# Kernel optimization log

Measured on AMD Instinct MI355X. Metric: run time of the kernel, lower is better.

Reference implementation:

```python
import jax, jax.numpy as jnp
import numpy as np
import math

K = 7
B, C, H, W = 16, 3, 256, 256
N = 50000
ANGLE = 30.0; TRANS = 0.45; SHEAR = 0.3; SCALE0, SCALE1 = 1.0, 0.5  # self.scale assumed [1.0,0.5] (upstream AutoDO)


def _bilinear(img, xs, ys):
    # img: (C,Hs,Ws); xs,ys: (Ho,Wo) pixel coords; border padding (clamp)
    Cc, Hs, Ws = img.shape
    xs = jnp.clip(xs, 0.0, Ws - 1.0)
    ys = jnp.clip(ys, 0.0, Hs - 1.0)
    x0 = jnp.floor(xs); y0 = jnp.floor(ys)
    wx = xs - x0; wy = ys - y0
    x0i = x0.astype(jnp.int32); y0i = y0.astype(jnp.int32)
    x1i = jnp.minimum(x0i + 1, Ws - 1); y1i = jnp.minimum(y0i + 1, Hs - 1)
    Ia = img[:, y0i, x0i]; Ib = img[:, y0i, x1i]
    Ic = img[:, y1i, x0i]; Id = img[:, y1i, x1i]
    return Ia * (1 - wx) * (1 - wy) + Ib * wx * (1 - wy) + Ic * (1 - wx) * wy + Id * wx * wy


def _resize(x, Ho, Wo):
    # torch F.interpolate bilinear, align_corners=False, no antialias
    Bb, Cc, Hs, Ws = x.shape
    ys = (jnp.arange(Ho, dtype=x.dtype) + 0.5) * (Hs / Ho) - 0.5
    xs = (jnp.arange(Wo, dtype=x.dtype) + 0.5) * (Ws / Wo) - 0.5
    Y, X = jnp.meshgrid(ys, xs, indexing='ij')
    return jax.vmap(lambda im: _bilinear(im, X, Y))(x)


def _warp_perspective(x, M, Ho, Wo):
    # kornia.warp_perspective: dst(p) = src(M^-1 p), bilinear, border padding, align_corners=True
    Bb, Cc, Hs, Ws = x.shape
    Minv = jnp.linalg.inv(M)  # (B,3,3)
    yy, xx = jnp.meshgrid(jnp.arange(Ho, dtype=x.dtype), jnp.arange(Wo, dtype=x.dtype), indexing='ij')
    pts = jnp.stack([xx.ravel(), yy.ravel(), jnp.ones(Ho * Wo, dtype=x.dtype)])  # (3, Ho*Wo)
    src = jnp.einsum('bij,jn->bin', Minv, pts)
    xs = (src[:, 0] / src[:, 2]).reshape(Bb, Ho, Wo)
    ys = (src[:, 1] / src[:, 2]).reshape(Bb, Ho, Wo)
    return jax.vmap(_bilinear)(x, xs, ys)


def _forward(x, paramP, paramM, gumbel_u, eps, idx):
    dt = x.dtype
    pP = jax.nn.sigmoid(paramP[:, idx])  # (K,B)
    logits = jnp.stack([jnp.log(pP).ravel(), jnp.log(1.0 - pP).ravel()], axis=1)  # (K*B,2)
    g = -jnp.log(-jnp.log(gumbel_u))
    y_soft = jax.nn.softmax(logits + g, axis=1)  # tau=1
    y_hard = jax.nn.one_hot(jnp.argmax(y_soft, axis=1), 2, dtype=y_soft.dtype)
    y = y_hard + y_soft - jax.lax.stop_gradient(y_soft)  # straight-through hard gumbel
    sP = y[:, 0].reshape(K, B)
    sM = jax.nn.sigmoid(paramM[:, idx]) * eps  # (K,B)
    ang = sP[0] * sM[0] * ANGLE
    # replicate torch's cat(W//2 * ones(B), H//2 * ones(B)).view(-1,2) layout exactly
    ctr = jnp.concatenate([jnp.full((B,), W // 2, dt), jnp.full((B,), H // 2, dt)]).reshape(-1, 2)
    sx = SCALE0 + sP[5] * sM[5] * SCALE1
    sy = SCALE0 + sP[6] * sM[6] * SCALE1
    rad = jnp.deg2rad(ang); ca = jnp.cos(rad); sa = jnp.sin(rad)
    # kornia get_rotation_matrix2d: rot=[[c,s],[-s,c]] @ diag(sx,sy); t = ctr - rot@ctr
    sr = jnp.stack([jnp.stack([ca * sx, sa * sy], -1), jnp.stack([-sa * sx, ca * sy], -1)], -2)  # (B,2,2)
    t = ctr - jnp.einsum('bij,bj->bi', sr, ctr)
    eye = jnp.broadcast_to(jnp.eye(3, dtype=dt), (B, 3, 3))
    R = eye.at[:, :2, :2].set(sr).at[:, :2, 2].set(t)
    T = eye.at[:, 0, 2].set(W * sP[1] * sM[1] * TRANS).at[:, 1, 2].set(H * sP[2] * sM[2] * TRANS)
    S = eye.at[:, 0, 1].set(sP[3] * sM[3] * SHEAR).at[:, 1, 0].set(sP[4] * sM[4] * SHEAR)
    M = S @ T @ R
    x_up = _resize(x, 4 * H, 4 * W)
    x_w = _warp_perspective(x_up, M, 4 * H, 4 * W)
    return _resize(x_w, H, W)


def setup_inputs() -> dict:
    key = jax.random.key(0)
    k1, k2, k3, k4 = jax.random.split(key, 4)
    p = 1.0 / (K - 2)
    prob_logit = math.log(p / (1.0 - p))
    m = 5.0 / 10.0
    magn_logit = math.log(m / (1.0 - m))
    return {
        'x': jax.random.uniform(k1, (B, C, H, W), jnp.float32),
        'paramP': jnp.full((K, N), prob_logit, jnp.float32),
        'paramM': jnp.full((K, N), magn_logit, jnp.float32),
        'gumbel_u': jax.random.uniform(k2, (K * B, 2), jnp.float32, minval=1e-6, maxval=1.0 - 1e-6),
        'eps': jax.random.normal(k3, (K, B), jnp.float32),
        'idx': jax.random.randint(k4, (B,), 0, N, jnp.int32),
    }


def reference(x, paramP, paramM, gumbel_u, eps, idx):
    return _forward(x, paramP, paramM, gumbel_u, eps, idx)
```

## Files before the change

kernel.cpp:

```cpp
#include <hip/hip_runtime.h>
#include <math.h>


typedef float floatx4 __attribute__((ext_vector_type(4)));

__device__ __forceinline__ floatx4 load4(const float* p) {
    floatx4 v;
    __builtin_memcpy(&v, p, sizeof(v));
    return v;
}

struct Up { int i0; float w; };

__device__ __forceinline__ Up upc(int v) {
    float u = fmaf(0.25f, (float)v, -0.375f);
    u = fminf(fmaxf(u, 0.0f), 255.0f);
    float f = floorf(u);
    Up r; r.i0 = (int)f; r.w = u - f;
    return r;
}

struct Trip { float w0, w1, w2; int base; };

__device__ __forceinline__ Trip merged3(float s) {
    float f = floorf(s);
    float fr = s - f;
    int v0 = (int)f;
    int v1 = min(v0 + 1, 1023);
    Up c0 = upc(v0), c1 = upc(v1);
    float A0 = 1.0f - fr, A1 = fr;
    float b0 = A1 * (1.0f - c1.w), b1 = A1 * c1.w;
    bool d = (c1.i0 != c0.i0);
    Trip t;
    t.w0 = A0 * (1.0f - c0.w) + (d ? 0.0f : b0);
    t.w1 = A0 * c0.w + (d ? b0 : b1);
    t.w2 = d ? b1 : 0.0f;
    t.base = c0.i0;
    return t;
}

__device__ __forceinline__ void pair_accum(
    Trip cA, Trip cB, Trip rA, Trip rB,
    const float* __restrict__ xb, float* acc)
{
    int cb = min(cA.base, cB.base);
    int rb = min(rA.base, rB.base);
    float CA[4], CB[4], RA[4], RB[4];
    bool sa_ = (cA.base != cb);
    CA[0] = sa_ ? 0.f : cA.w0;  CA[1] = sa_ ? cA.w0 : cA.w1;
    CA[2] = sa_ ? cA.w1 : cA.w2;  CA[3] = sa_ ? cA.w2 : 0.f;
    bool sb_ = (cB.base != cb);
    CB[0] = sb_ ? 0.f : cB.w0;  CB[1] = sb_ ? cB.w0 : cB.w1;
    CB[2] = sb_ ? cB.w1 : cB.w2;  CB[3] = sb_ ? cB.w2 : 0.f;
    bool ra_ = (rA.base != rb);
    RA[0] = ra_ ? 0.f : rA.w0;  RA[1] = ra_ ? rA.w0 : rA.w1;
    RA[2] = ra_ ? rA.w1 : rA.w2;  RA[3] = ra_ ? rA.w2 : 0.f;
    bool rb_ = (rB.base != rb);
    RB[0] = rb_ ? 0.f : rB.w0;  RB[1] = rb_ ? rB.w0 : rB.w1;
    RB[2] = rb_ ? rB.w1 : rB.w2;  RB[3] = rb_ ? rB.w2 : 0.f;

    float W[4][4];
#pragma unroll
    for (int r = 0; r < 4; ++r)
#pragma unroll
        for (int c = 0; c < 4; ++c)
            W[r][c] = fmaf(RB[r], CB[c], RA[r] * CA[c]);

    int base = cb;
    if (cb > 252) {
        int shift = cb - 252;
        base = 252;
        for (int s = 0; s < shift; ++s) {
#pragma unroll
            for (int r = 0; r < 4; ++r) {
                W[r][3] = W[r][2]; W[r][2] = W[r][1];
                W[r][1] = W[r][0]; W[r][0] = 0.f;
            }
        }
    }
    int e0 = rb * 256 + base;
    int e1 = min(rb + 1, 255) * 256 + base;
    int e2 = min(rb + 2, 255) * 256 + base;
    int e3 = min(rb + 3, 255) * 256 + base;
#pragma unroll
    for (int ch = 0; ch < 3; ++ch) {
        const float* pc = xb + ch * 65536;
        floatx4 L0 = load4(pc + e0);
        floatx4 L1 = load4(pc + e1);
        floatx4 L2 = load4(pc + e2);
        floatx4 L3 = load4(pc + e3);
        float s0 = fmaf(W[0][3], L0.w, fmaf(W[0][2], L0.z, fmaf(W[0][1], L0.y, W[0][0] * L0.x)));
        float s1 = fmaf(W[1][3], L1.w, fmaf(W[1][2], L1.z, fmaf(W[1][1], L1.y, W[1][0] * L1.x)));
        float s2 = fmaf(W[2][3], L2.w, fmaf(W[2][2], L2.z, fmaf(W[2][1], L2.y, W[2][0] * L2.x)));
        float s3 = fmaf(W[3][3], L3.w, fmaf(W[3][2], L3.z, fmaf(W[3][1], L3.y, W[3][0] * L3.x)));
        acc[ch] += (s0 + s1) + (s2 + s3);
    }
}

__global__ __launch_bounds__(256) void fused_warp(
    const float* __restrict__ x,
    const float* __restrict__ paramP, const float* __restrict__ paramM,
    const float* __restrict__ gumbel_u, const float* __restrict__ eps,
    const int* __restrict__ idx,
    float* __restrict__ out, int N)
{
    __shared__ float smem[8];

    int b = blockIdx.z;
    int tid = threadIdx.y * 16 + threadIdx.x;

    if (tid < 64) {
        float dec = 0.f, sMv = 0.f;
        if (tid < 7) {
            int k = tid;
            int id = idx[b];
            float vP = paramP[k * N + id];
            float pP = 1.0f / (1.0f + expf(-vP));
            float l0 = logf(pP);
            float l1 = logf(1.0f - pP);
            float u0 = gumbel_u[(k * 16 + b) * 2 + 0];
            float u1 = gumbel_u[(k * 16 + b) * 2 + 1];
            float g0 = -logf(-logf(u0));
            float g1 = -logf(-logf(u1));
            dec = (l0 + g0 >= l1 + g1) ? 1.0f : 0.0f;
            float vM = paramM[k * N + id];
            float sig = 1.0f / (1.0f + expf(-vM));
            sMv = sig * eps[k * 16 + b];
        }
        float sP[7], sM[7];
#pragma unroll
        for (int k = 0; k < 7; ++k) {
            sP[k] = __shfl(dec, k, 64);
            sM[k] = __shfl(sMv, k, 64);
        }
        if (tid == 0) {
            float ang = sP[0] * sM[0] * 30.0f;
            float rad = ang * 0.017453292519943295f;
            float ca = cosf(rad), sa = sinf(rad);
            float sx = 1.0f + sP[5] * sM[5] * 0.5f;
            float sy = 1.0f + sP[6] * sM[6] * 0.5f;
            float sr00 = ca * sx, sr01 = sa * sy;
            float sr10 = -sa * sx, sr11 = ca * sy;
            float t0 = 128.0f - (sr00 + sr01) * 128.0f;
            float t1 = 128.0f - (sr10 + sr11) * 128.0f;
            float tx2 = 256.0f * sP[1] * sM[1] * 0.45f;
            float ty2 = 256.0f * sP[2] * sM[2] * 0.45f;
            float sh01 = sP[3] * sM[3] * 0.3f;
            float sh10 = sP[4] * sM[4] * 0.3f;
            float e0 = t0 + tx2, e1 = t1 + ty2;
            float a  = sr00 + sh01 * sr10;
            float bb = sr01 + sh01 * sr11;
            float txm = e0 + sh01 * e1;
            float c  = sh10 * sr00 + sr10;
            float d  = sh10 * sr01 + sr11;
            float tym = sh10 * e0 + e1;
            float det = a * d - bb * c;
            float rdet = 1.0f / det;
            smem[0] = d * rdet;
            smem[1] = -bb * rdet;
            smem[2] = (bb * tym - d * txm) * rdet;
            smem[3] = -c * rdet;
            smem[4] = a * rdet;
            smem[5] = (c * txm - a * tym) * rdet;
        }
    }
    __syncthreads();

    float m00 = smem[0], m01 = smem[1], m02 = smem[2];
    float m10 = smem[3], m11 = smem[4], m12 = smem[5];

    int wid  = tid >> 6;
    int lane = tid & 63;
    int lx = lane & 7, ly = lane >> 3;
    int j = blockIdx.x * 16 + ((wid & 1) * 8 + lx);
    int i = blockIdx.y * 16 + ((wid >> 1) * 8 + ly);

    const float* xb = x + b * 3 * 65536;

    float XA = (float)(4 * j + 1);
    float Y0 = (float)(4 * i + 1);
    float x0 = fmaf(m00, XA, fmaf(m01, Y0, m02));
    float y0 = fmaf(m10, XA, fmaf(m11, Y0, m12));
    float xs[4], ys[4];
    xs[0] = x0;        ys[0] = y0;
    xs[1] = x0 + m00;  ys[1] = y0 + m10;
    xs[2] = x0 + m01;  ys[2] = y0 + m11;
    xs[3] = xs[1] + m01; ys[3] = ys[1] + m11;

    Trip cx[4], ry[4];
#pragma unroll
    for (int s = 0; s < 4; ++s) {
        cx[s] = merged3(fminf(fmaxf(xs[s], 0.f), 1023.f));
        ry[s] = merged3(fminf(fmaxf(ys[s], 0.f), 1023.f));
    }

    int cbmin = min(min(cx[0].base, cx[1].base), min(cx[2].base, cx[3].base));
    int cbmax = max(max(cx[0].base, cx[1].base), max(cx[2].base, cx[3].base));
    int rbmin = min(min(ry[0].base, ry[1].base), min(ry[2].base, ry[3].base));
    int rbmax = max(max(ry[0].base, ry[1].base), max(ry[2].base, ry[3].base));

    float acc[3] = {0.f, 0.f, 0.f};

    if (((cbmax - cbmin) | (rbmax - rbmin)) <= 1) {
        float W[4][4];
#pragma unroll
        for (int s = 0; s < 4; ++s) {
            bool sc = (cx[s].base != cbmin);
            float C0 = sc ? 0.f : cx[s].w0;
            float C1 = sc ? cx[s].w0 : cx[s].w1;
            float C2 = sc ? cx[s].w1 : cx[s].w2;
            float C3 = sc ? cx[s].w2 : 0.f;
            bool sr = (ry[s].base != rbmin);
            float R0 = sr ? 0.f : ry[s].w0;
            float R1 = sr ? ry[s].w0 : ry[s].w1;
            float R2 = sr ? ry[s].w1 : ry[s].w2;
            float R3 = sr ? ry[s].w2 : 0.f;
            float C[4] = {C0, C1, C2, C3};
            float R[4] = {R0, R1, R2, R3};
            if (s == 0) {
#pragma unroll
                for (int r = 0; r < 4; ++r)
#pragma unroll
                    for (int c = 0; c < 4; ++c)
                        W[r][c] = R[r] * C[c];
            } else {
#pragma unroll
                for (int r = 0; r < 4; ++r)
#pragma unroll
                    for (int c = 0; c < 4; ++c)
                        W[r][c] = fmaf(R[r], C[c], W[r][c]);
            }
        }

        int base = cbmin;
        if (cbmin > 252) {
            int shift = cbmin - 252;
            base = 252;
            for (int s = 0; s < shift; ++s) {
#pragma unroll
                for (int r = 0; r < 4; ++r) {
                    W[r][3] = W[r][2]; W[r][2] = W[r][1];
                    W[r][1] = W[r][0]; W[r][0] = 0.f;
                }
            }
        }

        int e0 = rbmin * 256 + base;
        int e1 = min(rbmin + 1, 255) * 256 + base;
        int e2 = min(rbmin + 2, 255) * 256 + base;
        int e3 = min(rbmin + 3, 255) * 256 + base;
#pragma unroll
        for (int ch = 0; ch < 3; ++ch) {
            const float* pc = xb + ch * 65536;
            floatx4 L0 = load4(pc + e0);
            floatx4 L1 = load4(pc + e1);
            floatx4 L2 = load4(pc + e2);
            floatx4 L3 = load4(pc + e3);
            float s0 = fmaf(W[0][3], L0.w, fmaf(W[0][2], L0.z, fmaf(W[0][1], L0.y, W[0][0] * L0.x)));
            float s1 = fmaf(W[1][3], L1.w, fmaf(W[1][2], L1.z, fmaf(W[1][1], L1.y, W[1][0] * L1.x)));
            float s2 = fmaf(W[2][3], L2.w, fmaf(W[2][2], L2.z, fmaf(W[2][1], L2.y, W[2][0] * L2.x)));
            float s3 = fmaf(W[3][3], L3.w, fmaf(W[3][2], L3.z, fmaf(W[3][1], L3.y, W[3][0] * L3.x)));
            acc[ch] = (s0 + s1) + (s2 + s3);
        }
    } else {
        pair_accum(cx[0], cx[1], ry[0], ry[1], xb, acc);
        pair_accum(cx[2], cx[3], ry[2], ry[3], xb, acc);
    }

    int obase = ((b * 3) * 256 + i) * 256 + j;
    out[obase]          = 0.25f * acc[0];
    out[obase + 65536]  = 0.25f * acc[1];
    out[obase + 131072] = 0.25f * acc[2];
}

extern "C" void kernel_launch(void* const* d_in, const int* in_sizes, int n_in,
                              void* d_out, int out_size, void* d_ws, size_t ws_size,
                              hipStream_t stream) {
    const float* x      = (const float*)d_in[0];
    const float* paramP = (const float*)d_in[1];
    const float* paramM = (const float*)d_in[2];
    const float* gumbel = (const float*)d_in[3];
    const float* eps    = (const float*)d_in[4];
    const int*   idx    = (const int*)d_in[5];
    float* out = (float*)d_out;
    int N = in_sizes[1] / 7;

    hipLaunchKernelGGL(fused_warp, dim3(16, 16, 16), dim3(16, 16, 1), 0, stream,
                       x, paramP, paramM, gumbel, eps, idx, out, N);
}
```

Before: 89.31 us.

## Stage per-block source bounding box in LDS before bilinear gather

Thread 0 now computes the bounding box of source pixels a 16x16 output tile will touch under the inverse affine map. If the box fits, the whole block cooperatively copies it for all three channels into shared memory. The 4x4 gathers then read from LDS instead of global memory, with a fallback to the old global path. This adds a second barrier, about 36KB of LDS per block (which may lower occupancy), and scalar LDS reads that replace the vectorised global loads.

```diff
diff --git a/kernel.cpp b/kernel.cpp
--- a/kernel.cpp
+++ b/kernel.cpp
@@ -3,6 +3,8 @@
 
 
 typedef float floatx4 __attribute__((ext_vector_type(4)));
+
+#define LDS_CH 3072
 
 __device__ __forceinline__ floatx4 load4(const float* p) {
     floatx4 v;
@@ -39,9 +41,18 @@
     return t;
 }
 
-__device__ __forceinline__ void pair_accum(
+__device__ __forceinline__ int basefun(float s) {
+    s = fminf(fmaxf(s, 0.f), 1023.f);
+    float f = floorf(s);
+    int v0 = (int)f;
+    float u = fmaf(0.25f, (float)v0, -0.375f);
+    u = fminf(fmaxf(u, 0.0f), 255.0f);
+    return (int)floorf(u);
+}
+
+__device__ __forceinline__ void pair_weights(
     Trip cA, Trip cB, Trip rA, Trip rB,
-    const float* __restrict__ xb, float* acc)
+    float W[4][4], int* cb_out, int* rb_out, int* base_out)
 {
     int cb = min(cA.base, cB.base);
     int rb = min(rA.base, rB.base);
@@ -59,7 +70,6 @@
     RB[0] = rb_ ? 0.f : rB.w0;  RB[1] = rb_ ? rB.w0 : rB.w1;
     RB[2] = rb_ ? rB.w1 : rB.w2;  RB[3] = rb_ ? rB.w2 : 0.f;
 
-    float W[4][4];
 #pragma unroll
     for (int r = 0; r < 4; ++r)
 #pragma unroll
@@ -78,6 +88,15 @@
             }
         }
     }
+    *cb_out = cb; *rb_out = rb; *base_out = base;
+}
+
+__device__ __forceinline__ void pair_accum(
+    Trip cA, Trip cB, Trip rA, Trip rB,
+    const float* __restrict__ xb, float* acc)
+{
+    float W[4][4]; int cb, rb, base;
+    pair_weights(cA, cB, rA, rB, W, &cb, &rb, &base);
     int e0 = rb * 256 + base;
     int e1 = min(rb + 1, 255) * 256 + base;
     int e2 = min(rb + 2, 255) * 256 + base;
@@ -97,6 +116,32 @@
     }
 }
 
+__device__ __forceinline__ void pair_accum_lds(
+    Trip cA, Trip cB, Trip rA, Trip rB,
+    const float* lds0, int Wp, int r0, int c0, float* acc)
+{
+    float W[4][4]; int cb, rb, base;
+    pair_weights(cA, cB, rA, rB, W, &cb, &rb, &base);
+    int lb = base - c0;
+    int l0 = (rb - r0) * Wp + lb;
+    int l1 = (min(rb + 1, 255) - r0) * Wp + lb;
+    int l2 = (min(rb + 2, 255) - r0) * Wp + lb;
+    int l3 = (min(rb + 3, 255) - r0) * Wp + lb;
+#pragma unroll
+    for (int ch = 0; ch < 3; ++ch) {
+        const float* pc = lds0 + ch * LDS_CH;
+        float L0x = pc[l0], L0y = pc[l0+1], L0z = pc[l0+2], L0w = pc[l0+3];
+        float L1x = pc[l1], L1y = pc[l1+1], L1z = pc[l1+2], L1w = pc[l1+3];
+        float L2x = pc[l2], L2y = pc[l2+1], L2z = pc[l2+2], L2w = pc[l2+3];
+        float L3x = pc[l3], L3y = pc[l3+1], L3z = pc[l3+2], L3w = pc[l3+3];
+        float s0 = fmaf(W[0][3], L0w, fmaf(W[0][2], L0z, fmaf(W[0][1], L0y, W[0][0] * L0x)));
+        float s1 = fmaf(W[1][3], L1w, fmaf(W[1][2], L1z, fmaf(W[1][1], L1y, W[1][0] * L1x)));
+        float s2 = fmaf(W[2][3], L2w, fmaf(W[2][2], L2z, fmaf(W[2][1], L2y, W[2][0] * L2x)));
+        float s3 = fmaf(W[3][3], L3w, fmaf(W[3][2], L3z, fmaf(W[3][1], L3y, W[3][0] * L3x)));
+        acc[ch] += (s0 + s1) + (s2 + s3);
+    }
+}
+
 __global__ __launch_bounds__(256) void fused_warp(
     const float* __restrict__ x,
     const float* __restrict__ paramP, const float* __restrict__ paramM,
@@ -105,6 +150,8 @@
     float* __restrict__ out, int N)
 {
     __shared__ float smem[8];
+    __shared__ int sbox[8];
+    __shared__ float lds[3 * LDS_CH];
 
     int b = blockIdx.z;
     int tid = threadIdx.y * 16 + threadIdx.x;
@@ -156,18 +203,74 @@
             float tym = sh10 * e0 + e1;
             float det = a * d - bb * c;
             float rdet = 1.0f / det;
-            smem[0] = d * rdet;
-            smem[1] = -bb * rdet;
-            smem[2] = (bb * tym - d * txm) * rdet;
-            smem[3] = -c * rdet;
-            smem[4] = a * rdet;
-            smem[5] = (c * txm - a * tym) * rdet;
+            float im00 = d * rdet;
+            float im01 = -bb * rdet;
+            float im02 = (bb * tym - d * txm) * rdet;
+            float im10 = -c * rdet;
+            float im11 = a * rdet;
+            float im12 = (c * txm - a * tym) * rdet;
+            smem[0] = im00; smem[1] = im01; smem[2] = im02;
+            smem[3] = im10; smem[4] = im11; smem[5] = im12;
+
+            float XA0 = (float)(4 * (blockIdx.x * 16) + 1);
+            float Y00 = (float)(4 * (blockIdx.y * 16) + 1);
+            float XA1 = XA0 + 60.0f;
+            float Y01 = Y00 + 60.0f;
+
+            float inxlo = fmaf(im01, (im01 >= 0.f ? Y00 : Y01), im02);
+            float inxhi = fmaf(im01, (im01 >= 0.f ? Y01 : Y00), im02);
+            float xlo = fmaf(im00, (im00 >= 0.f ? XA0 : XA1), inxlo);
+            float xhi = fmaf(im00, (im00 >= 0.f ? XA1 : XA0), inxhi);
+            float xl1 = xlo + im00, xl2 = xlo + im01, xl3 = xl1 + im01;
+            float xh1 = xhi + im00, xh2 = xhi + im01, xh3 = xh1 + im01;
+            float xsl = fminf(fminf(xlo, xl1), fminf(xl2, xl3));
+            float xsh = fmaxf(fmaxf(xhi, xh1), fmaxf(xh2, xh3));
+
+            float inylo = fmaf(im11, (im11 >= 0.f ? Y00 : Y01), im12);
+            float inyhi = fmaf(im11, (im11 >= 0.f ? Y01 : Y00), im12);
+            float ylo = fmaf(im10, (im10 >= 0.f ? XA0 : XA1), inylo);
+            float yhi = fmaf(im10, (im10 >= 0.f ? XA1 : XA0), inyhi);
+            float yl1 = ylo + im10, yl2 = ylo + im11, yl3 = yl1 + im11;
+            float yh1 = yhi + im10, yh2 = yhi + im11, yh3 = yh1 + im11;
+            float ysl = fminf(fminf(ylo, yl1), fminf(yl2, yl3));
+            float ysh = fmaxf(fmaxf(yhi, yh1), fmaxf(yh2, yh3));
+
+            int c0 = min(basefun(xsl), 252);
+            int c1 = min(basefun(xsh) + 3, 255);
+            int r0 = basefun(ysl);
+            int r1 = min(basefun(ysh) + 3, 255);
+            int wB = c1 - c0 + 1, hB = r1 - r0 + 1;
+            int Wp = wB | 1;
+            int fits = (wB <= 64) && (Wp * hB <= LDS_CH);
+            sbox[0] = c0; sbox[1] = r0; sbox[2] = Wp; sbox[3] = hB;
+            sbox[4] = fits; sbox[5] = wB;
         }
     }
     __syncthreads();
 
     float m00 = smem[0], m01 = smem[1], m02 = smem[2];
     float m10 = smem[3], m11 = smem[4], m12 = smem[5];
+    int c0 = sbox[0], r0 = sbox[1], Wp = sbox[2], hB = sbox[3];
+    int fits = sbox[4], wB = sbox[5];
+
+    const float* xb = x + b * 3 * 65536;
+
+    if (fits) {
+        int cc = tid & 63;
+        int rr = tid >> 6;
+        for (int r = rr; r < hB; r += 4) {
+            if (cc < wB) {
+                const float* src = xb + (r0 + r) * 256 + c0 + cc;
+                float v0 = src[0];
+                float v1 = src[65536];
+                float v2 = src[131072];
+                int di = r * Wp + cc;
+                lds[di]              = v0;
+                lds[LDS_CH + di]     = v1;
+                lds[2 * LDS_CH + di] = v2;
+            }
+        }
+    }
 
     int wid  = tid >> 6;
     int lane = tid & 63;
@@ -175,16 +278,14 @@
     int j = blockIdx.x * 16 + ((wid & 1) * 8 + lx);
     int i = blockIdx.y * 16 + ((wid >> 1) * 8 + ly);
 
-    const float* xb = x + b * 3 * 65536;
-
     float XA = (float)(4 * j + 1);
     float Y0 = (float)(4 * i + 1);
     float x0 = fmaf(m00, XA, fmaf(m01, Y0, m02));
     float y0 = fmaf(m10, XA, fmaf(m11, Y0, m12));
     float xs[4], ys[4];
-    xs[0] = x0;        ys[0] = y0;
-    xs[1] = x0 + m00;  ys[1] = y0 + m10;
-    xs[2] = x0 + m01;  ys[2] = y0 + m11;
+    xs[0] = x0;          ys[0] = y0;
+    xs[1] = x0 + m00;    ys[1] = y0 + m10;
+    xs[2] = x0 + m01;    ys[2] = y0 + m11;
     xs[3] = xs[1] + m01; ys[3] = ys[1] + m11;
 
     Trip cx[4], ry[4];
@@ -198,6 +299,8 @@
     int cbmax = max(max(cx[0].base, cx[1].base), max(cx[2].base, cx[3].base));
     int rbmin = min(min(ry[0].base, ry[1].base), min(ry[2].base, ry[3].base));
     int rbmax = max(max(ry[0].base, ry[1].base), max(ry[2].base, ry[3].base));
+
+    __syncthreads();
 
     float acc[3] = {0.f, 0.f, 0.f};
 
@@ -245,26 +348,57 @@
             }
         }
 
-        int e0 = rbmin * 256 + base;
-        int e1 = min(rbmin + 1, 255) * 256 + base;
-        int e2 = min(rbmin + 2, 255) * 256 + base;
-        int e3 = min(rbmin + 3, 255) * 256 + base;
-#pragma unroll
-        for (int ch = 0; ch < 3; ++ch) {
-            const float* pc = xb + ch * 65536;
-            floatx4 L0 = load4(pc + e0);
-            floatx4 L1 = load4(pc + e1);
-            floatx4 L2 = load4(pc + e2);
-            floatx4 L3 = load4(pc + e3);
-            float s0 = fmaf(W[0][3], L0.w, fmaf(W[0][2], L0.z, fmaf(W[0][1], L0.y, W[0][0] * L0.x)));
-            float s1 = fmaf(W[1][3], L1.w, fmaf(W[1][2], L1.z, fmaf(W[1][1], L1.y, W[1][0] * L1.x)));
-            float s2 = fmaf(W[2][3], L2.w, fmaf(W[2][2], L2.z, fmaf(W[2][1], L2.y, W[2][0] * L2.x)));
-            float s3 = fmaf(W[3][3], L3.w, fmaf(W[3][2], L3.z, fmaf(W[3][1], L3.y, W[3][0] * L3.x)));
-            acc[ch] = (s0 + s1) + (s2 + s3);
+        int g0 = rbmin;
+        int g1 = min(rbmin + 1, 255);
+        int g2 = min(rbmin + 2, 255);
+        int g3 = min(rbmin + 3, 255);
+
+        if (fits) {
+            int lb = base - c0;
+            int l0 = (g0 - r0) * Wp + lb;
+            int l1 = (g1 - r0) * Wp + lb;
+            int l2 = (g2 - r0) * Wp + lb;
+            int l3 = (g3 - r0) * Wp + lb;
+#pragma unroll
+            for (int ch = 0; ch < 3; ++ch) {
+                const float* pc = lds + ch * LDS_CH;
+                float L0x = pc[l0], L0y = pc[l0+1], L0z = pc[l0+2], L0w = pc[l0+3];
+                float L1x = pc[l1], L1y = pc[l1+1], L1z = pc[l1+2], L1w = pc[l1+3];
+                float L2x = pc[l2], L2y = pc[l2+1], L2z = pc[l2+2], L2w = pc[l2+3];
+                float L3x = pc[l3], L3y = pc[l3+1], L3z = pc[l3+2], L3w = pc[l3+3];
+                float s0 = fmaf(W[0][3], L0w, fmaf(W[0][2], L0z, fmaf(W[0][1], L0y, W[0][0] * L0x)));
+                float s1 = fmaf(W[1][3], L1w, fmaf(W[1][2], L1z, fmaf(W[1][1], L1y, W[1][0] * L1x)));
+                float s2 = fmaf(W[2][3], L2w, fmaf(W[2][2], L2z, fmaf(W[2][1], L2y, W[2][0] * L2x)));
+                float s3 = fmaf(W[3][3], L3w, fmaf(W[3][2], L3z, fmaf(W[3][1], L3y, W[3][0] * L3x)));
+                acc[ch] = (s0 + s1) + (s2 + s3);
+            }
+        } else {
+            int e0 = g0 * 256 + base;
+            int e1 = g1 * 256 + base;
+            int e2 = g2 * 256 + base;
+            int e3 = g3 * 256 + base;
+#pragma unroll
+            for (int ch = 0; ch < 3; ++ch) {
+                const float* pc = xb + ch * 65536;
+                floatx4 L0 = load4(pc + e0);
+                floatx4 L1 = load4(pc + e1);
+                floatx4 L2 = load4(pc + e2);
+                floatx4 L3 = load4(pc + e3);
+                float s0 = fmaf(W[0][3], L0.w, fmaf(W[0][2], L0.z, fmaf(W[0][1], L0.y, W[0][0] * L0.x)));
+                float s1 = fmaf(W[1][3], L1.w, fmaf(W[1][2], L1.z, fmaf(W[1][1], L1.y, W[1][0] * L1.x)));
+                float s2 = fmaf(W[2][3], L2.w, fmaf(W[2][2], L2.z, fmaf(W[2][1], L2.y, W[2][0] * L2.x)));
+                float s3 = fmaf(W[3][3], L3.w, fmaf(W[3][2], L3.z, fmaf(W[3][1], L3.y, W[3][0] * L3.x)));
+                acc[ch] = (s0 + s1) + (s2 + s3);
+            }
         }
     } else {
-        pair_accum(cx[0], cx[1], ry[0], ry[1], xb, acc);
-        pair_accum(cx[2], cx[3], ry[2], ry[3], xb, acc);
+        if (fits) {
+            pair_accum_lds(cx[0], cx[1], ry[0], ry[1], lds, Wp, r0, c0, acc);
+            pair_accum_lds(cx[2], cx[3], ry[2], ry[3], lds, Wp, r0, c0, acc);
+        } else {
+            pair_accum(cx[0], cx[1], ry[0], ry[1], xb, acc);
+            pair_accum(cx[2], cx[3], ry[2], ry[3], xb, acc);
+        }
     }
 
     int obase = ((b * 3) * 256 + i) * 256 + j;
```

Measured after the change: 99.19 us. 1.11x slower.

## Iterate fast-path bilinear rows over wave-uniform range with per-lane predication

Applied to the files above, without the earlier changes.

Restructures the fast gather path so each wave loops over a row range that is the same for every lane. The range comes from wave-wide min/max shuffle reductions and readfirstlane. Each lane uses only the rows that fall in its own 4-row window and selects its weight row by offset. The aim is uniform control flow and loop-based loads, but it adds 12 shuffle reductions and may loop over many more rows than 4 when source rows vary widely across a wave, as they do under rotation and shear.

```diff
diff --git a/kernel.cpp b/kernel.cpp
--- a/kernel.cpp
+++ b/kernel.cpp
@@ -37,6 +37,24 @@
     t.w2 = d ? b1 : 0.0f;
     t.base = c0.i0;
     return t;
+}
+
+__device__ __forceinline__ int wave_min_i(int v) {
+#pragma unroll
+    for (int m = 1; m < 64; m <<= 1) {
+        int o = __shfl_xor(v, m, 64);
+        v = min(v, o);
+    }
+    return v;
+}
+
+__device__ __forceinline__ int wave_max_i(int v) {
+#pragma unroll
+    for (int m = 1; m < 64; m <<= 1) {
+        int o = __shfl_xor(v, m, 64);
+        v = max(v, o);
+    }
+    return v;
 }
 
 __device__ __forceinline__ void pair_accum(
@@ -199,70 +217,95 @@
     int rbmin = min(min(ry[0].base, ry[1].base), min(ry[2].base, ry[3].base));
     int rbmax = max(max(ry[0].base, ry[1].base), max(ry[2].base, ry[3].base));
 
-    float acc[3] = {0.f, 0.f, 0.f};
-
-    if (((cbmax - cbmin) | (rbmax - rbmin)) <= 1) {
-        float W[4][4];
-#pragma unroll
-        for (int s = 0; s < 4; ++s) {
-            bool sc = (cx[s].base != cbmin);
-            float C0 = sc ? 0.f : cx[s].w0;
-            float C1 = sc ? cx[s].w0 : cx[s].w1;
-            float C2 = sc ? cx[s].w1 : cx[s].w2;
-            float C3 = sc ? cx[s].w2 : 0.f;
-            bool sr = (ry[s].base != rbmin);
-            float R0 = sr ? 0.f : ry[s].w0;
-            float R1 = sr ? ry[s].w0 : ry[s].w1;
-            float R2 = sr ? ry[s].w1 : ry[s].w2;
-            float R3 = sr ? ry[s].w2 : 0.f;
-            float C[4] = {C0, C1, C2, C3};
-            float R[4] = {R0, R1, R2, R3};
-            if (s == 0) {
-#pragma unroll
-                for (int r = 0; r < 4; ++r)
-#pragma unroll
-                    for (int c = 0; c < 4; ++c)
-                        W[r][c] = R[r] * C[c];
-            } else {
-#pragma unroll
-                for (int r = 0; r < 4; ++r)
-#pragma unroll
-                    for (int c = 0; c < 4; ++c)
-                        W[r][c] = fmaf(R[r], C[c], W[r][c]);
+    bool fastl = (((cbmax - cbmin) | (rbmax - rbmin)) <= 1);
+
+    float W[4][4];
+#pragma unroll
+    for (int s = 0; s < 4; ++s) {
+        bool sc = (cx[s].base != cbmin);
+        float C0 = sc ? 0.f : cx[s].w0;
+        float C1 = sc ? cx[s].w0 : cx[s].w1;
+        float C2 = sc ? cx[s].w1 : cx[s].w2;
+        float C3 = sc ? cx[s].w2 : 0.f;
+        bool sr = (ry[s].base != rbmin);
+        float R0 = sr ? 0.f : ry[s].w0;
+        float R1 = sr ? ry[s].w0 : ry[s].w1;
+        float R2 = sr ? ry[s].w1 : ry[s].w2;
+        float R3 = sr ? ry[s].w2 : 0.f;
+        float C[4] = {C0, C1, C2, C3};
+        float R[4] = {R0, R1, R2, R3};
+        if (s == 0) {
+#pragma unroll
+            for (int r = 0; r < 4; ++r)
+#pragma unroll
+                for (int c = 0; c < 4; ++c)
+                    W[r][c] = R[r] * C[c];
+        } else {
+#pragma unroll
+            for (int r = 0; r < 4; ++r)
+#pragma unroll
+                for (int c = 0; c < 4; ++c)
+                    W[r][c] = fmaf(R[r], C[c], W[r][c]);
+        }
+    }
+
+    int base = cbmin;
+    if (cbmin > 252) {
+        int shift = cbmin - 252;
+        base = 252;
+        for (int s = 0; s < shift; ++s) {
+#pragma unroll
+            for (int r = 0; r < 4; ++r) {
+                W[r][3] = W[r][2]; W[r][2] = W[r][1];
+                W[r][1] = W[r][0]; W[r][0] = 0.f;
             }
         }
-
-        int base = cbmin;
-        if (cbmin > 252) {
-            int shift = cbmin - 252;
-            base = 252;
-            for (int s = 0; s < shift; ++s) {
-#pragma unroll
-                for (int r = 0; r < 4; ++r) {
-                    W[r][3] = W[r][2]; W[r][2] = W[r][1];
-                    W[r][1] = W[r][0]; W[r][0] = 0.f;
-                }
-            }
-        }
-
-        int e0 = rbmin * 256 + base;
-        int e1 = min(rbmin + 1, 255) * 256 + base;
-        int e2 = min(rbmin + 2, 255) * 256 + base;
-        int e3 = min(rbmin + 3, 255) * 256 + base;
-#pragma unroll
-        for (int ch = 0; ch < 3; ++ch) {
-            const float* pc = xb + ch * 65536;
-            floatx4 L0 = load4(pc + e0);
-            floatx4 L1 = load4(pc + e1);
-            floatx4 L2 = load4(pc + e2);
-            floatx4 L3 = load4(pc + e3);
-            float s0 = fmaf(W[0][3], L0.w, fmaf(W[0][2], L0.z, fmaf(W[0][1], L0.y, W[0][0] * L0.x)));
-            float s1 = fmaf(W[1][3], L1.w, fmaf(W[1][2], L1.z, fmaf(W[1][1], L1.y, W[1][0] * L1.x)));
-            float s2 = fmaf(W[2][3], L2.w, fmaf(W[2][2], L2.z, fmaf(W[2][1], L2.y, W[2][0] * L2.x)));
-            float s3 = fmaf(W[3][3], L3.w, fmaf(W[3][2], L3.z, fmaf(W[3][1], L3.y, W[3][0] * L3.x)));
-            acc[ch] = (s0 + s1) + (s2 + s3);
-        }
-    } else {
+    }
+
+    int rb = rbmin;
+    int rlo = wave_min_i(fastl ? rb : 255);
+    int rhi = wave_max_i(fastl ? rb : -4) + 3;
+    rlo = __builtin_amdgcn_readfirstlane(rlo);
+    rhi = __builtin_amdgcn_readfirstlane(min(rhi, 255));
+
+    const float* p0 = xb;
+    const float* p1 = xb + 65536;
+    const float* p2 = xb + 131072;
+
+    float a01_0 = 0.f, a23_0 = 0.f;
+    float a01_1 = 0.f, a23_1 = 0.f;
+    float a01_2 = 0.f, a23_2 = 0.f;
+
+    int e = rlo * 256 + base;
+    int d = rlo - rb;
+    for (int r = rlo; r <= rhi; ++r) {
+        if ((unsigned)d <= 3u) {
+            bool q0 = (d == 0), q2 = (d == 2);
+            bool lo2 = (d < 2);
+            float w0 = lo2 ? (q0 ? W[0][0] : W[1][0]) : (q2 ? W[2][0] : W[3][0]);
+            float w1 = lo2 ? (q0 ? W[0][1] : W[1][1]) : (q2 ? W[2][1] : W[3][1]);
+            float w2 = lo2 ? (q0 ? W[0][2] : W[1][2]) : (q2 ? W[2][2] : W[3][2]);
+            float w3 = lo2 ? (q0 ? W[0][3] : W[1][3]) : (q2 ? W[2][3] : W[3][3]);
+            floatx4 L0 = load4(p0 + e);
+            floatx4 L1 = load4(p1 + e);
+            floatx4 L2 = load4(p2 + e);
+            float v0 = fmaf(w3, L0.w, fmaf(w2, L0.z, fmaf(w1, L0.y, w0 * L0.x)));
+            float v1 = fmaf(w3, L1.w, fmaf(w2, L1.z, fmaf(w1, L1.y, w0 * L1.x)));
+            float v2 = fmaf(w3, L2.w, fmaf(w2, L2.z, fmaf(w1, L2.y, w0 * L2.x)));
+            a01_0 += lo2 ? v0 : 0.f;  a23_0 += lo2 ? 0.f : v0;
+            a01_1 += lo2 ? v1 : 0.f;  a23_1 += lo2 ? 0.f : v1;
+            a01_2 += lo2 ? v2 : 0.f;  a23_2 += lo2 ? 0.f : v2;
+        }
+        e += 256;
+        ++d;
+    }
+
+    float acc[3];
+    acc[0] = fastl ? (a01_0 + a23_0) : 0.f;
+    acc[1] = fastl ? (a01_1 + a23_1) : 0.f;
+    acc[2] = fastl ? (a01_2 + a23_2) : 0.f;
+
+    if (!fastl) {
         pair_accum(cx[0], cx[1], ry[0], ry[1], xb, acc);
         pair_accum(cx[2], cx[3], ry[2], ry[3], xb, acc);
     }
```

Result: slower. 106.2 us (+18.9%).
